# Kernel tuning notes

Measured on AMD Instinct MI355X. Metric: run time of the kernel, lower is better.

Reference implementation:

```python
import jax, jax.numpy as jnp
import numpy as np

EPS = 1e-5
PATCH_SIZES = [None, 13]
PATCH_WEIGHTS = [0.5, 0.5]


def _box(x, p):
    # sliding-window sum over spatial dims, VALID padding -> [B,C,H-p+1,W-p+1]
    return jax.lax.reduce_window(x, 0.0, jax.lax.add, (1, 1, p, p), (1, 1, 1, 1), 'VALID')


def _global_ncc(x1, x2):
    # InstanceNorm2d (biased var, eps) per (b,c) over spatial dims, then dot / (c*h*w)
    b, c, h, w = x1.shape
    m1 = jnp.mean(x1, axis=(2, 3), keepdims=True)
    m2 = jnp.mean(x2, axis=(2, 3), keepdims=True)
    v1 = jnp.mean((x1 - m1) ** 2, axis=(2, 3), keepdims=True)
    v2 = jnp.mean((x2 - m2) ** 2, axis=(2, 3), keepdims=True)
    n1 = (x1 - m1) * jax.lax.rsqrt(v1 + EPS)
    n2 = (x2 - m2) * jax.lax.rsqrt(v2 + EPS)
    return jnp.sum(n1 * n2, axis=(1, 2, 3)) / (c * h * w)


def _patch_ncc(x1, x2, p):
    # Equivalent fused form of: unfold -> rearrange (patch locations become
    # channels, pxp patch pixels become spatial) -> InstanceNorm2d -> dot.
    # Each pxp patch is normalized over its own pixels => local NCC.
    b, c, h, w = x1.shape
    n = p * p
    s1 = _box(x1, p)
    s2 = _box(x2, p)
    s11 = _box(x1 * x1, p)
    s22 = _box(x2 * x2, p)
    s12 = _box(x1 * x2, p)
    m1 = s1 / n
    m2 = s2 / n
    v1 = s11 / n - m1 * m1  # biased variance, matches InstanceNorm2d
    v2 = s22 / n - m2 * m2
    cross = s12 - n * m1 * m2  # sum_p (I-mI)(J-mJ)
    cc = cross * jax.lax.rsqrt((v1 + EPS) * (v2 + EPS))  # [B,C,H',W']
    hp, wp = h - p + 1, w - p + 1
    # original divides by (channels' * h' * w') where channels' = c*hp*wp, spatial = p*p
    return jnp.sum(cc, axis=(1, 2, 3)) / (c * hp * wp * n)


def setup_inputs() -> dict:
    key = jax.random.key(0)
    k1, k2 = jax.random.split(key)
    x1 = jax.random.normal(k1, (32, 1, 512, 512), dtype=jnp.float32)
    x2 = jax.random.normal(k2, (32, 1, 512, 512), dtype=jnp.float32)
    return {"x1": x1, "x2": x2}


def reference(x1, x2):
    scores = []
    for w, p in zip(PATCH_WEIGHTS, PATCH_SIZES):
        if p is None:
            scores.append(w * _global_ncc(x1, x2))
        else:
            scores.append(w * _patch_ncc(x1, x2, p))
    return jnp.stack(scores, axis=0).sum(axis=0)  # [B]
```

## Files before the change

### kernel.cpp

```cpp
#include <hip/hip_runtime.h>

#define EPS 1e-5f

typedef float v2f __attribute__((ext_vector_type(2)));

constexpr int B = 32;
constexpr int H = 512;
constexpr int W = 512;
constexpr int NPIX = H * W;
constexpr int P = 13;
constexpr int HP = H - P + 1;
constexpr int WP = W - P + 1;
constexpr int TILES_X = 8;
constexpr int BAND_OUT = 40;
constexpr int BANDS_Y = 13;
constexpr int G = 13;
constexpr int NGROUPS = 4;
constexpr int ITER_LAST_OWN = 20;
constexpr int ITER_LAST_EMIT = 32;
constexpr int BLOCKS_PER_B = TILES_X * BANDS_Y;
constexpr int RS = 76;

#define GLOAD_LDS16(gp, lp)                                                    \
  __builtin_amdgcn_global_load_lds(                                            \
      (const __attribute__((address_space(1))) unsigned int*)(const void*)(gp),\
      (__attribute__((address_space(3))) unsigned int*)(void*)(lp), 16, 0, 0)

__global__ __launch_bounds__(64) void ncc_fused_kernel(
    const float* __restrict__ x1, const float* __restrict__ x2,
    float* __restrict__ part) {
  const int bid = blockIdx.x;
  const int b    = bid / BLOCKS_PER_B;
  const int rem  = bid % BLOCKS_PER_B;
  const int tile = rem % TILES_X;
  const int band = rem / TILES_X;
  const bool last = (band == BANDS_Y - 1);
  const int x0 = tile * 64;
  const int y0 = last ? (HP - BAND_OUT) : band * BAND_OUT;
  const int tid = threadIdx.x;
  const int c0 = x0 + tid;
  const bool valid = c0 < WP;

  __shared__ float sa[2][G][RS];
  __shared__ float sb[2][G][RS];

  const float* r1 = x1 + (size_t)b * NPIX + (size_t)y0 * W + x0;
  const float* r2 = x2 + (size_t)b * NPIX + (size_t)y0 * W + x0;

  int qoff = tid * 4;
  { int mx = W - x0 - 4; if (qoff > mx) qoff = mx; }
  const bool loader = tid < 19;

  auto stage = [&](int g, int buf) {
    if (loader) {
#pragma unroll
      for (int r = 0; r < G; ++r) {
        GLOAD_LDS16(r1 + (size_t)(g * G + r) * W + qoff, &sa[buf][r][0]);
        GLOAD_LDS16(r2 + (size_t)(g * G + r) * W + qoff, &sb[buf][r][0]);
      }
    }
  };

  float rr1[G], rr2[G], rr11[G], rr22[G], rr12[G];
  float S1 = 0.f, S2 = 0.f, S11 = 0.f, S22 = 0.f, S12 = 0.f;
  float g1 = 0.f, g2 = 0.f, g11 = 0.f, g22 = 0.f, g12 = 0.f;
  float acc = 0.f;
  const float inv_n = 1.0f / 169.0f;

  auto step = [&](int u, int buf, int t, bool fill) {
    const float* pa = &sa[buf][u][tid];
    const float* pb = &sb[buf][u][tid];
    v2f A2[6], B2[6];
#pragma unroll
    for (int j = 0; j < 6; ++j) {
      A2[j] = (v2f){pa[2 * j], pa[2 * j + 1]};
      B2[j] = (v2f){pb[2 * j], pb[2 * j + 1]};
    }
    float a12 = pa[12], b12 = pb[12];

    v2f q11 = A2[0] * A2[0], q22 = B2[0] * B2[0], q12 = A2[0] * B2[0];
    v2f h1v = A2[0], h2v = B2[0], h11v = q11, h22v = q22, h12v = q12;
#pragma unroll
    for (int j = 1; j < 6; ++j) {
      h1v += A2[j];
      h2v += B2[j];
      h11v += A2[j] * A2[j];
      h22v += B2[j] * B2[j];
      h12v += A2[j] * B2[j];
    }
    float h1 = h1v.x + h1v.y + a12;
    float h2 = h2v.x + h2v.y + b12;
    float h11 = fmaf(a12, a12, h11v.x + h11v.y);
    float h22 = fmaf(b12, b12, h22v.x + h22v.y);
    float h12 = fmaf(a12, b12, h12v.x + h12v.y);

    bool owned = last ? (t >= ITER_LAST_OWN) : (t < BAND_OUT);
    if (owned) {
      g1 += A2[0].x; g2 += B2[0].x;
      g11 += q11.x; g22 += q22.x; g12 += q12.x;
    }

    if (fill) {
      S1 += h1; S2 += h2; S11 += h11; S22 += h22; S12 += h12;
    } else {
      S1 += h1 - rr1[u]; S2 += h2 - rr2[u];
      S11 += h11 - rr11[u]; S22 += h22 - rr22[u]; S12 += h12 - rr12[u];
    }
    rr1[u] = h1; rr2[u] = h2; rr11[u] = h11; rr22[u] = h22; rr12[u] = h12;

    bool do_out = (t >= 12) && (!last || t >= ITER_LAST_EMIT);
    if (do_out) {
      float m1 = S1 * inv_n, m2 = S2 * inv_n;
      float vv1 = fmaf(-m1, m1, S11 * inv_n) + EPS;
      float vv2 = fmaf(-m2, m2, S22 * inv_n) + EPS;
      float cross = fmaf(-m1, S2, S12);
      float cc = cross * rsqrtf(vv1 * vv2);
      acc += valid ? cc : 0.f;
    }
  };

  stage(0, 0);
  __syncthreads();
  stage(1, 1);

#pragma unroll
  for (int u = 0; u < G; ++u) step(u, 0, u, true);
  __syncthreads();

#pragma clang loop unroll(disable)
  for (int g = 1; g < NGROUPS; ++g) {
    if (g + 1 < NGROUPS) stage(g + 1, (g + 1) & 1);
    const int buf = g & 1;
#pragma unroll
    for (int u = 0; u < G; ++u) step(u, buf, g * G + u, false);
    __syncthreads();
  }

  float v0 = acc;
  float w1 = g1, w2 = g2, w3 = g11, w4 = g22, w5 = g12;
#pragma unroll
  for (int off = 32; off > 0; off >>= 1) {
    v0 += __shfl_down(v0, off, 64);
    w1 += __shfl_down(w1, off, 64);
    w2 += __shfl_down(w2, off, 64);
    w3 += __shfl_down(w3, off, 64);
    w4 += __shfl_down(w4, off, 64);
    w5 += __shfl_down(w5, off, 64);
  }
  if (tid == 0) {
    float* o = part + (size_t)bid * 6;
    o[0] = v0; o[1] = w1; o[2] = w2; o[3] = w3; o[4] = w4; o[5] = w5;
  }
}

__global__ __launch_bounds__(64) void final_kernel(
    const float* __restrict__ part, float* __restrict__ out) {
  int b = blockIdx.x;
  int tid = threadIdx.x;
  float s[6] = {0.f, 0.f, 0.f, 0.f, 0.f, 0.f};
  for (int i = tid; i < BLOCKS_PER_B; i += 64) {
    const float* p = part + (size_t)(b * BLOCKS_PER_B + i) * 6;
#pragma unroll
    for (int k = 0; k < 6; ++k) s[k] += p[k];
  }
#pragma unroll
  for (int off = 32; off > 0; off >>= 1) {
#pragma unroll
    for (int k = 0; k < 6; ++k) s[k] += __shfl_down(s[k], off, 64);
  }
  if (tid == 0) {
    float Nf = (float)NPIX;
    float m1 = s[1] / Nf;
    float m2 = s[2] / Nf;
    float v1 = fmaf(-m1, m1, s[3] / Nf);
    float v2 = fmaf(-m2, m2, s[4] / Nf);
    float cross = fmaf(-Nf * m1, m2, s[5]);
    float g = cross * rsqrtf((v1 + EPS) * (v2 + EPS)) / Nf;
    float patch = s[0] / ((float)HP * (float)WP * 169.0f);
    out[b] = 0.5f * g + 0.5f * patch;
  }
}

extern "C" void kernel_launch(void* const* d_in, const int* in_sizes, int n_in,
                              void* d_out, int out_size, void* d_ws, size_t ws_size,
                              hipStream_t stream) {
  const float* x1 = (const float*)d_in[0];
  const float* x2 = (const float*)d_in[1];
  float* out = (float*)d_out;
  float* part = (float*)d_ws;

  ncc_fused_kernel<<<B * BLOCKS_PER_B, 64, 0, stream>>>(x1, x2, part);
  final_kernel<<<B, 64, 0, stream>>>(part, out);
}
```

Baseline: 127.6 us.

## Replace double-buffered group staging with per-row ring buffer and vmcnt waits

Drops the two-buffer group staging and its block-wide barriers. A 13-row LDS ring is used instead: after each row is read, the load for the row 13 ahead is issued into the freed slot, and a waitcnt on outstanding vector memory ops gates consumption. This halves LDS use and removes __syncthreads, which fits a single-wave block. The correctness of this fine-grained pipelining depends on the counter arithmetic and the LDS-read wait. Redundant clamped loads at the tail add a little extra traffic.

```diff
diff --git a/kernel.cpp b/kernel.cpp
--- a/kernel.cpp
+++ b/kernel.cpp
@@ -15,6 +15,7 @@
 constexpr int BAND_OUT = 40;
 constexpr int BANDS_Y = 13;
 constexpr int G = 13;
+constexpr int NROWS = 52;
 constexpr int NGROUPS = 4;
 constexpr int ITER_LAST_OWN = 20;
 constexpr int ITER_LAST_EMIT = 32;
@@ -41,8 +42,8 @@
   const int c0 = x0 + tid;
   const bool valid = c0 < WP;
 
-  __shared__ float sa[2][G][RS];
-  __shared__ float sb[2][G][RS];
+  __shared__ float sa[G][RS];
+  __shared__ float sb[G][RS];
 
   const float* r1 = x1 + (size_t)b * NPIX + (size_t)y0 * W + x0;
   const float* r2 = x2 + (size_t)b * NPIX + (size_t)y0 * W + x0;
@@ -51,15 +52,15 @@
   { int mx = W - x0 - 4; if (qoff > mx) qoff = mx; }
   const bool loader = tid < 19;
 
-  auto stage = [&](int g, int buf) {
+  auto dma_row = [&](int row, int slot) {
     if (loader) {
-#pragma unroll
-      for (int r = 0; r < G; ++r) {
-        GLOAD_LDS16(r1 + (size_t)(g * G + r) * W + qoff, &sa[buf][r][0]);
-        GLOAD_LDS16(r2 + (size_t)(g * G + r) * W + qoff, &sb[buf][r][0]);
-      }
+      GLOAD_LDS16(r1 + (size_t)row * W + qoff, &sa[slot][0]);
+      GLOAD_LDS16(r2 + (size_t)row * W + qoff, &sb[slot][0]);
     }
   };
+
+#pragma unroll
+  for (int r = 0; r < G; ++r) dma_row(r, r);
 
   float rr1[G], rr2[G], rr11[G], rr22[G], rr12[G];
   float S1 = 0.f, S2 = 0.f, S11 = 0.f, S22 = 0.f, S12 = 0.f;
@@ -67,9 +68,10 @@
   float acc = 0.f;
   const float inv_n = 1.0f / 169.0f;
 
-  auto step = [&](int u, int buf, int t, bool fill) {
-    const float* pa = &sa[buf][u][tid];
-    const float* pb = &sb[buf][u][tid];
+  auto step = [&](int u, int t, bool fill) {
+    asm volatile("s_waitcnt vmcnt(24)" ::: "memory");
+    const float* pa = &sa[u][tid];
+    const float* pb = &sb[u][tid];
     v2f A2[6], B2[6];
 #pragma unroll
     for (int j = 0; j < 6; ++j) {
@@ -77,6 +79,12 @@
       B2[j] = (v2f){pb[2 * j], pb[2 * j + 1]};
     }
     float a12 = pa[12], b12 = pb[12];
+    asm volatile("s_waitcnt lgkmcnt(0)" ::: "memory");
+    {
+      int nrow = t + G;
+      if (nrow > NROWS - 1) nrow = NROWS - 1;
+      dma_row(nrow, u);
+    }
 
     v2f q11 = A2[0] * A2[0], q22 = B2[0] * B2[0], q12 = A2[0] * B2[0];
     v2f h1v = A2[0], h2v = B2[0], h11v = q11, h22v = q22, h12v = q12;
@@ -119,22 +127,16 @@
     }
   };
 
-  stage(0, 0);
-  __syncthreads();
-  stage(1, 1);
-
 #pragma unroll
-  for (int u = 0; u < G; ++u) step(u, 0, u, true);
-  __syncthreads();
+  for (int u = 0; u < G; ++u) step(u, u, true);
 
 #pragma clang loop unroll(disable)
   for (int g = 1; g < NGROUPS; ++g) {
-    if (g + 1 < NGROUPS) stage(g + 1, (g + 1) & 1);
-    const int buf = g & 1;
 #pragma unroll
-    for (int u = 0; u < G; ++u) step(u, buf, g * G + u, false);
-    __syncthreads();
+    for (int u = 0; u < G; ++u) step(u, g * G + u, false);
   }
+
+  asm volatile("s_waitcnt vmcnt(0)" ::: "memory");
 
   float v0 = acc;
   float w1 = g1, w2 = g2, w3 = g11, w4 = g22, w5 = g12;
```

Result: slower. 144.5 us (+13.3%).
